# Kernel optimization log

Hardware: AMD Instinct MI355X
Metric: run time of the kernel (lower is better)

## Reference

```python
import jax, jax.numpy as jnp
import numpy as np

B, H, T, D = 2, 16, 2048, 64
BASE_WINDOW = 256
FULL = 999999


def _make_window_sizes(num_heads=H, base_window=BASE_WINDOW):
    ws = []
    for h in range(num_heads):
        if h < num_heads // 4:
            ws.append(base_window)
        elif h < num_heads // 2:
            ws.append(base_window * 2)
        elif h < 3 * num_heads // 4:
            ws.append(base_window * 4)
        else:
            ws.append(FULL)
    return jnp.asarray(ws, dtype=jnp.int32)


def setup_inputs() -> dict:
    key = jax.random.key(0)
    kq, kk, kv = jax.random.split(key, 3)
    Q = jax.random.normal(kq, (B, H, T, D), dtype=jnp.float32)
    K = jax.random.normal(kk, (B, H, T, D), dtype=jnp.float32)
    V = jax.random.normal(kv, (B, H, T, D), dtype=jnp.float32)
    return {"Q": Q, "K": K, "V": V, "window_sizes": _make_window_sizes()}


def reference(Q, K, V, window_sizes):
    b, h, t, d = Q.shape
    scale = 1.0 / np.sqrt(d).astype(np.float32)
    idx = jnp.arange(t, dtype=jnp.int32)
    diff = idx[:, None] - idx[None, :]  # [T, T], q_idx - kv_idx
    # causal & |q-k| <= w  ==  0 <= diff <= w  (per head)
    mask = (diff >= 0) & (diff[None, :, :] <= window_sizes[:, None, None])  # [H, T, T]
    scores = jnp.einsum('bhqd,bhkd->bhqk', Q, K) * scale  # [B, H, T, T]
    scores = jnp.where(mask[None], scores, -jnp.inf)
    attn = jax.nn.softmax(scores, axis=-1)
    return jnp.einsum('bhqk,bhkd->bhqd', attn, V)
```

## Files before the change

kernel.cpp:

```cpp
#include <hip/hip_runtime.h>
#include <hip/hip_bf16.h>


constexpr int Bc = 2, Hc = 16, Tc = 2048, Dc = 64;
constexpr int BQ = 64;
constexpr int BK = 32;
constexpr float QSCALE = 0.125f * 1.44269504088896340736f;
constexpr float CMAX = 16.0f;

constexpr size_t KB_OFF = 256;
constexpr size_t VB_OFF = 256 + (size_t)Bc * Hc * Tc * Dc * 2;
constexpr int HEADE = Tc * Dc;

typedef __attribute__((ext_vector_type(8))) short short8;
typedef __attribute__((ext_vector_type(4))) float float4v;
typedef __attribute__((ext_vector_type(2))) unsigned int uint2v;

#if defined(__has_builtin)
#if __has_builtin(__builtin_amdgcn_exp2f)
#define EXP2 __builtin_amdgcn_exp2f
#endif
#endif
#ifndef EXP2
#define EXP2 exp2f
#endif

__device__ inline unsigned f2bf_u(float f) {
    union { float f; unsigned u; } v; v.f = f;
    return (v.u + 0x7fffu + ((v.u >> 16) & 1u)) >> 16;
}

__device__ inline short8 pack8(const float* t) {
    short8 r;
#pragma unroll
    for (int j = 0; j < 8; j++) r[j] = (short)f2bf_u(t[j]);
    return r;
}

__device__ inline unsigned pk_bf16(float a, float b) {
    __hip_bfloat162 h = __float22bfloat162_rn(make_float2(a, b));
    union { __hip_bfloat162 h; unsigned u; } v; v.h = h;
    return v.u;
}

__device__ inline short8 mk8(unsigned a0, unsigned a1, unsigned a2, unsigned a3) {
    union { unsigned u[4]; short8 s; } v;
    v.u[0] = a0; v.u[1] = a1; v.u[2] = a2; v.u[3] = a3;
    return v.s;
}

__global__ __launch_bounds__(256)
void preconv_kernel(const float* __restrict__ K, const float* __restrict__ V,
                    unsigned short* __restrict__ Kb, unsigned short* __restrict__ Vtb) {
    const int blk = blockIdx.x;
    const int tid = threadIdx.x;
    if (blk < 2048) {
        const int base = blk * 2048 + tid * 8;
        float4v a = *(const float4v*)(K + base);
        float4v b = *(const float4v*)(K + base + 4);
        float t[8] = {a[0], a[1], a[2], a[3], b[0], b[1], b[2], b[3]};
        *(short8*)(Kb + base) = pack8(t);
    } else {
        __shared__ float tile[64][65];
        const int blk2 = blk - 2048;
        const int bh = blk2 >> 5;
        const int t0 = (blk2 & 31) * 64;
        const float* src = V + (size_t)bh * HEADE + (size_t)t0 * Dc;
#pragma unroll
        for (int i = 0; i < 4; i++) {
            const int r = (tid >> 4) + i * 16;
            const int d4 = (tid & 15) * 4;
            float4v v4 = *(const float4v*)(src + r * Dc + d4);
            tile[r][d4] = v4[0]; tile[r][d4 + 1] = v4[1];
            tile[r][d4 + 2] = v4[2]; tile[r][d4 + 3] = v4[3];
        }
        __syncthreads();
        unsigned short* dst = Vtb + (size_t)bh * HEADE + t0;
#pragma unroll
        for (int i = 0; i < 2; i++) {
            const int d = (tid >> 3) + 32 * i;
            const int c = tid & 7;
            float t[8];
#pragma unroll
            for (int j = 0; j < 8; j++) t[j] = tile[c * 8 + j][d];
            *(short8*)(dst + (size_t)d * Tc + c * 8) = pack8(t);
        }
    }
}

__global__ __launch_bounds__(256, 4)
void dswa_kernel(const float* __restrict__ Q,
                 const unsigned short* __restrict__ Kb,
                 const unsigned short* __restrict__ Vtb,
                 const int* __restrict__ wsz,
                 float* __restrict__ O) {
    __shared__ __align__(16) unsigned short LDS[18432];

    const int tid  = threadIdx.x;
    const int wave = tid >> 6;
    const int g    = wave >> 1;
    const int wq   = wave & 1;
    const int lane = tid & 63;
    const int quad = lane >> 4;
    const int l16  = lane & 15;

    unsigned short* Kw = &LDS[wave * 4608];
    unsigned short* Vw = &LDS[wave * 4608 + 2048];

    const int krow  = lane >> 1;
    const int kcolh = (lane & 1) * 32;
    const int vrow  = lane;

    const int blk  = blockIdx.x;
    const int ci   = blk & 255;
    const int slot = blk >> 8;
    const int b    = ci & 1;
    const int q5   = (ci >> 1) & 31;
    const int hh   = ci >> 6;
    const int h    = (3 - slot) * 4 + hh;
    const int qt   = (slot == 0) ? q5 : 31 - q5;
    const int q0   = qt * BQ;
    const int win  = wsz[h];

    const size_t headoff = (size_t)(b * Hc + h) * HEADE;
    const float* Qp = Q + headoff;
    const unsigned short* Kbh = Kb + headoff;
    const unsigned short* Vbh = Vtb + headoff;
    float* Op = O + headoff;

    short8 qf[2][2];
#pragma unroll
    for (int s = 0; s < 2; s++) {
        const int qrow = q0 + wq * 32 + s * 16 + l16;
#pragma unroll
        for (int c = 0; c < 2; c++) {
            const float* src = Qp + (size_t)qrow * Dc + c * 32 + quad * 8;
            float4v a = *(const float4v*)src;
            float4v d4 = *(const float4v*)(src + 4);
            float t[8] = {a[0]*QSCALE, a[1]*QSCALE, a[2]*QSCALE, a[3]*QSCALE,
                          d4[0]*QSCALE, d4[1]*QSCALE, d4[2]*QSCALE, d4[3]*QSCALE};
            qf[s][c] = pack8(t);
        }
    }

    float4v acc[2][4];
#pragma unroll
    for (int s = 0; s < 2; s++)
#pragma unroll
        for (int nb = 0; nb < 4; nb++) acc[s][nb] = (float4v){0.f, 0.f, 0.f, 0.f};
    float lp0 = 0.0f, lp1 = 0.0f;

    const int kv_lo = (max(0, q0 - win)) & ~(BK - 1);
    const int C = (q0 + BQ - kv_lo) >> 5;

    const int kv0g = kv_lo + g * BK;
    const unsigned short* kgp = Kbh + (size_t)(kv0g + krow) * Dc + kcolh;
    const unsigned short* vgp = Vbh + (size_t)vrow * Tc + kv0g;

    short8 kr0, kr1, kr2, kr3, vr0, vr1, vr2, vr3;
    if (g < C) {
        kr0 = *(const short8*)(kgp);
        kr1 = *(const short8*)(kgp + 8);
        kr2 = *(const short8*)(kgp + 16);
        kr3 = *(const short8*)(kgp + 24);
        vr0 = *(const short8*)(vgp);
        vr1 = *(const short8*)(vgp + 8);
        vr2 = *(const short8*)(vgp + 16);
        vr3 = *(const short8*)(vgp + 24);
    }
    kgp += 64 * Dc; vgp += 64;

    for (int ti = g; ti < C; ti += 2) {
        const int kv0 = kv_lo + ti * BK;

        {
            const int ks = (krow & 7) << 3;
            *(short8*)&Kw[krow * 64 + ((kcolh)      ^ ks)] = kr0;
            *(short8*)&Kw[krow * 64 + ((kcolh + 8)  ^ ks)] = kr1;
            *(short8*)&Kw[krow * 64 + ((kcolh + 16) ^ ks)] = kr2;
            *(short8*)&Kw[krow * 64 + ((kcolh + 24) ^ ks)] = kr3;
            *(short8*)&Vw[vrow * 40 + 0]  = vr0;
            *(short8*)&Vw[vrow * 40 + 8]  = vr1;
            *(short8*)&Vw[vrow * 40 + 16] = vr2;
            *(short8*)&Vw[vrow * 40 + 24] = vr3;
        }

        if (ti + 2 < C) {
            kr0 = *(const short8*)(kgp);
            kr1 = *(const short8*)(kgp + 8);
            kr2 = *(const short8*)(kgp + 16);
            kr3 = *(const short8*)(kgp + 24);
            vr0 = *(const short8*)(vgp);
            vr1 = *(const short8*)(vgp + 8);
            vr2 = *(const short8*)(vgp + 16);
            vr3 = *(const short8*)(vgp + 24);
        }
        kgp += 64 * Dc; vgp += 64;

        float4v sT0[2], sT1[2];
        __builtin_amdgcn_s_setprio(1);
#pragma unroll
        for (int mb = 0; mb < 2; mb++) {
            float4v c0 = {-CMAX, -CMAX, -CMAX, -CMAX};
            float4v c1 = {-CMAX, -CMAX, -CMAX, -CMAX};
#pragma unroll
            for (int ch = 0; ch < 2; ch++) {
                const int row = mb * 16 + l16;
                short8 kf = *(short8*)&Kw[row * 64 +
                                          ((ch * 32 + quad * 8) ^ ((row & 7) << 3))];
                c0 = __builtin_amdgcn_mfma_f32_16x16x32_bf16(kf, qf[0][ch], c0, 0, 0, 0);
                c1 = __builtin_amdgcn_mfma_f32_16x16x32_bf16(kf, qf[1][ch], c1, 0, 0, 0);
            }
            sT0[mb] = c0; sT1[mb] = c1;
        }
        __builtin_amdgcn_s_setprio(0);

        short8 pf0, pf1;
        {
            const int rs = q0 + wq * 32;
            const bool interior = (kv0 + 31 <= rs) && (rs + 15 - kv0 <= win);
            if (!interior) {
                const int dbase = rs + l16 - kv0 - quad * 4;
#pragma unroll
                for (int mb = 0; mb < 2; mb++)
#pragma unroll
                    for (int r = 0; r < 4; r++) {
                        const unsigned diff = (unsigned)(dbase - mb * 16 - r);
                        sT0[mb][r] = (diff <= (unsigned)win) ? sT0[mb][r] : -3.0e38f;
                    }
            }
            unsigned w[4];
#pragma unroll
            for (int mb = 0; mb < 2; mb++) {
                float p0 = EXP2(sT0[mb][0]);
                float p1 = EXP2(sT0[mb][1]);
                float p2 = EXP2(sT0[mb][2]);
                float p3 = EXP2(sT0[mb][3]);
                lp0 += (p0 + p1) + (p2 + p3);
                w[2 * mb]     = pk_bf16(p0, p1);
                w[2 * mb + 1] = pk_bf16(p2, p3);
            }
            uint2v pa = __builtin_amdgcn_permlane32_swap(w[0], w[2], false, false);
            uint2v c02 = __builtin_amdgcn_permlane16_swap(pa[0], pa[1], false, false);
            uint2v pb = __builtin_amdgcn_permlane32_swap(w[1], w[3], false, false);
            uint2v c13 = __builtin_amdgcn_permlane16_swap(pb[0], pb[1], false, false);
            pf0 = mk8(c02[0], c13[0], c02[1], c13[1]);
        }
        {
            const int rs = q0 + wq * 32 + 16;
            const bool interior = (kv0 + 31 <= rs) && (rs + 15 - kv0 <= win);
            if (!interior) {
                const int dbase = rs + l16 - kv0 - quad * 4;
#pragma unroll
                for (int mb = 0; mb < 2; mb++)
#pragma unroll
                    for (int r = 0; r < 4; r++) {
                        const unsigned diff = (unsigned)(dbase - mb * 16 - r);
                        sT1[mb][r] = (diff <= (unsigned)win) ? sT1[mb][r] : -3.0e38f;
                    }
            }
            unsigned w[4];
#pragma unroll
            for (int mb = 0; mb < 2; mb++) {
                float p0 = EXP2(sT1[mb][0]);
                float p1 = EXP2(sT1[mb][1]);
                float p2 = EXP2(sT1[mb][2]);
                float p3 = EXP2(sT1[mb][3]);
                lp1 += (p0 + p1) + (p2 + p3);
                w[2 * mb]     = pk_bf16(p0, p1);
                w[2 * mb + 1] = pk_bf16(p2, p3);
            }
            uint2v pa = __builtin_amdgcn_permlane32_swap(w[0], w[2], false, false);
            uint2v c02 = __builtin_amdgcn_permlane16_swap(pa[0], pa[1], false, false);
            uint2v pb = __builtin_amdgcn_permlane32_swap(w[1], w[3], false, false);
            uint2v c13 = __builtin_amdgcn_permlane16_swap(pb[0], pb[1], false, false);
            pf1 = mk8(c02[0], c13[0], c02[1], c13[1]);
        }

        __builtin_amdgcn_s_setprio(1);
#pragma unroll
        for (int nb = 0; nb < 4; nb++) {
            short8 vf = *(short8*)&Vw[(nb * 16 + l16) * 40 + quad * 8];
            acc[0][nb] = __builtin_amdgcn_mfma_f32_16x16x32_bf16(pf0, vf, acc[0][nb], 0, 0, 0);
            acc[1][nb] = __builtin_amdgcn_mfma_f32_16x16x32_bf16(pf1, vf, acc[1][nb], 0, 0, 0);
        }
        __builtin_amdgcn_s_setprio(0);
    }

    lp0 += __shfl_xor(lp0, 16); lp0 += __shfl_xor(lp0, 32);
    lp1 += __shfl_xor(lp1, 16); lp1 += __shfl_xor(lp1, 32);

    __syncthreads();
    float* fl = (float*)LDS;
    if (g == 1) {
#pragma unroll
        for (int s = 0; s < 2; s++) {
            if (quad == 0) fl[(wq * 32 + s * 16 + l16) * 66 + 64] = (s ? lp1 : lp0);
#pragma unroll
            for (int r = 0; r < 4; r++) {
                const int row = wq * 32 + s * 16 + quad * 4 + r;
#pragma unroll
                for (int nb = 0; nb < 4; nb++)
                    fl[row * 66 + nb * 16 + l16] = acc[s][nb][r];
            }
        }
    }
    __syncthreads();
    if (g == 0) {
#pragma unroll
        for (int s = 0; s < 2; s++) {
            const float lps = s ? lp1 : lp0;
#pragma unroll
            for (int r = 0; r < 4; r++) {
                const int row = wq * 32 + s * 16 + quad * 4 + r;
                const float l0 = __shfl(lps, quad * 4 + r);
                const float lt = l0 + fl[row * 66 + 64];
                const float inv = 1.0f / lt;
                float* dst = Op + (size_t)(q0 + row) * Dc;
#pragma unroll
                for (int nb = 0; nb < 4; nb++)
                    dst[nb * 16 + l16] = (acc[s][nb][r] + fl[row * 66 + nb * 16 + l16]) * inv;
            }
        }
    }
}

extern "C" void kernel_launch(void* const* d_in, const int* in_sizes, int n_in,
                              void* d_out, int out_size, void* d_ws, size_t ws_size,
                              hipStream_t stream) {
    (void)in_sizes; (void)n_in; (void)ws_size; (void)out_size;
    const float* Q = (const float*)d_in[0];
    const float* K = (const float*)d_in[1];
    const float* V = (const float*)d_in[2];
    const int* wsz = (const int*)d_in[3];
    float* Out = (float*)d_out;

    unsigned short* Kb  = (unsigned short*)((char*)d_ws + KB_OFF);
    unsigned short* Vtb = (unsigned short*)((char*)d_ws + VB_OFF);

    preconv_kernel<<<dim3(3072), dim3(256), 0, stream>>>(K, V, Kb, Vtb);
    dswa_kernel<<<dim3(1024), dim3(256), 0, stream>>>(Q, Kb, Vtb, wsz, Out);
}
```

Baseline: 140.1 us.

## Load K and V MFMA fragments directly from global memory, bypassing LDS

Drops the per-wave LDS staging of K and V tiles. MFMA operand fragments are now loaded straight from global memory (K prefetched one iteration ahead, V loaded right after the QK MFMAs), and LDS shrinks to just the final reduction buffer. This removes the LDS write/read round trip and its latency, and the smaller LDS footprint may allow higher occupancy. In exchange the global loads are smaller and less coalesced (16-byte pieces scattered across rows), and V load latency is now exposed inside the iteration rather than hidden by a full-tile prefetch.

Result: no change. 141.0 us (+0.6%).

```diff
diff --git a/kernel.cpp b/kernel.cpp
--- a/kernel.cpp
+++ b/kernel.cpp
@@ -94,7 +94,7 @@
                  const unsigned short* __restrict__ Vtb,
                  const int* __restrict__ wsz,
                  float* __restrict__ O) {
-    __shared__ __align__(16) unsigned short LDS[18432];
+    __shared__ __align__(16) float fl[4224];
 
     const int tid  = threadIdx.x;
     const int wave = tid >> 6;
@@ -103,13 +103,6 @@
     const int lane = tid & 63;
     const int quad = lane >> 4;
     const int l16  = lane & 15;
-
-    unsigned short* Kw = &LDS[wave * 4608];
-    unsigned short* Vw = &LDS[wave * 4608 + 2048];
-
-    const int krow  = lane >> 1;
-    const int kcolh = (lane & 1) * 32;
-    const int vrow  = lane;
 
     const int blk  = blockIdx.x;
     const int ci   = blk & 255;
@@ -153,67 +146,51 @@
     const int kv_lo = (max(0, q0 - win)) & ~(BK - 1);
     const int C = (q0 + BQ - kv_lo) >> 5;
 
-    const int kv0g = kv_lo + g * BK;
-    const unsigned short* kgp = Kbh + (size_t)(kv0g + krow) * Dc + kcolh;
-    const unsigned short* vgp = Vbh + (size_t)vrow * Tc + kv0g;
-
-    short8 kr0, kr1, kr2, kr3, vr0, vr1, vr2, vr3;
-    if (g < C) {
-        kr0 = *(const short8*)(kgp);
-        kr1 = *(const short8*)(kgp + 8);
-        kr2 = *(const short8*)(kgp + 16);
-        kr3 = *(const short8*)(kgp + 24);
-        vr0 = *(const short8*)(vgp);
-        vr1 = *(const short8*)(vgp + 8);
-        vr2 = *(const short8*)(vgp + 16);
-        vr3 = *(const short8*)(vgp + 24);
-    }
-    kgp += 64 * Dc; vgp += 64;
+    const unsigned short* kbase = Kbh + (size_t)l16 * Dc + quad * 8;
+    const unsigned short* vbase = Vbh + (size_t)l16 * Tc + quad * 8;
+
+    short8 k0, k1, k2, k3;
+    {
+        const unsigned short* kp = kbase + (size_t)(kv_lo + g * BK) * Dc;
+        k0 = *(const short8*)(kp);
+        k1 = *(const short8*)(kp + 16 * Dc);
+        k2 = *(const short8*)(kp + 32);
+        k3 = *(const short8*)(kp + 16 * Dc + 32);
+    }
 
     for (int ti = g; ti < C; ti += 2) {
         const int kv0 = kv_lo + ti * BK;
 
-        {
-            const int ks = (krow & 7) << 3;
-            *(short8*)&Kw[krow * 64 + ((kcolh)      ^ ks)] = kr0;
-            *(short8*)&Kw[krow * 64 + ((kcolh + 8)  ^ ks)] = kr1;
-            *(short8*)&Kw[krow * 64 + ((kcolh + 16) ^ ks)] = kr2;
-            *(short8*)&Kw[krow * 64 + ((kcolh + 24) ^ ks)] = kr3;
-            *(short8*)&Vw[vrow * 40 + 0]  = vr0;
-            *(short8*)&Vw[vrow * 40 + 8]  = vr1;
-            *(short8*)&Vw[vrow * 40 + 16] = vr2;
-            *(short8*)&Vw[vrow * 40 + 24] = vr3;
-        }
-
-        if (ti + 2 < C) {
-            kr0 = *(const short8*)(kgp);
-            kr1 = *(const short8*)(kgp + 8);
-            kr2 = *(const short8*)(kgp + 16);
-            kr3 = *(const short8*)(kgp + 24);
-            vr0 = *(const short8*)(vgp);
-            vr1 = *(const short8*)(vgp + 8);
-            vr2 = *(const short8*)(vgp + 16);
-            vr3 = *(const short8*)(vgp + 24);
-        }
-        kgp += 64 * Dc; vgp += 64;
-
         float4v sT0[2], sT1[2];
         __builtin_amdgcn_s_setprio(1);
-#pragma unroll
-        for (int mb = 0; mb < 2; mb++) {
+        {
             float4v c0 = {-CMAX, -CMAX, -CMAX, -CMAX};
-            float4v c1 = {-CMAX, -CMAX, -CMAX, -CMAX};
-#pragma unroll
-            for (int ch = 0; ch < 2; ch++) {
-                const int row = mb * 16 + l16;
-                short8 kf = *(short8*)&Kw[row * 64 +
-                                          ((ch * 32 + quad * 8) ^ ((row & 7) << 3))];
-                c0 = __builtin_amdgcn_mfma_f32_16x16x32_bf16(kf, qf[0][ch], c0, 0, 0, 0);
-                c1 = __builtin_amdgcn_mfma_f32_16x16x32_bf16(kf, qf[1][ch], c1, 0, 0, 0);
-            }
-            sT0[mb] = c0; sT1[mb] = c1;
+            float4v c1 = c0, c2 = c0, c3 = c0;
+            c0 = __builtin_amdgcn_mfma_f32_16x16x32_bf16(k0, qf[0][0], c0, 0, 0, 0);
+            c1 = __builtin_amdgcn_mfma_f32_16x16x32_bf16(k0, qf[1][0], c1, 0, 0, 0);
+            c2 = __builtin_amdgcn_mfma_f32_16x16x32_bf16(k1, qf[0][0], c2, 0, 0, 0);
+            c3 = __builtin_amdgcn_mfma_f32_16x16x32_bf16(k1, qf[1][0], c3, 0, 0, 0);
+            c0 = __builtin_amdgcn_mfma_f32_16x16x32_bf16(k2, qf[0][1], c0, 0, 0, 0);
+            c1 = __builtin_amdgcn_mfma_f32_16x16x32_bf16(k2, qf[1][1], c1, 0, 0, 0);
+            c2 = __builtin_amdgcn_mfma_f32_16x16x32_bf16(k3, qf[0][1], c2, 0, 0, 0);
+            c3 = __builtin_amdgcn_mfma_f32_16x16x32_bf16(k3, qf[1][1], c3, 0, 0, 0);
+            sT0[0] = c0; sT1[0] = c1; sT0[1] = c2; sT1[1] = c3;
         }
         __builtin_amdgcn_s_setprio(0);
+
+        const unsigned short* vp = vbase + kv0;
+        short8 vf0 = *(const short8*)(vp);
+        short8 vf1 = *(const short8*)(vp + 16 * Tc);
+        short8 vf2 = *(const short8*)(vp + 32 * Tc);
+        short8 vf3 = *(const short8*)(vp + 48 * Tc);
+
+        if (ti + 2 < C) {
+            const unsigned short* kp = kbase + (size_t)(kv0 + 2 * BK) * Dc;
+            k0 = *(const short8*)(kp);
+            k1 = *(const short8*)(kp + 16 * Dc);
+            k2 = *(const short8*)(kp + 32);
+            k3 = *(const short8*)(kp + 16 * Dc + 32);
+        }
 
         short8 pf0, pf1;
         {
@@ -278,12 +255,14 @@
         }
 
         __builtin_amdgcn_s_setprio(1);
-#pragma unroll
-        for (int nb = 0; nb < 4; nb++) {
-            short8 vf = *(short8*)&Vw[(nb * 16 + l16) * 40 + quad * 8];
-            acc[0][nb] = __builtin_amdgcn_mfma_f32_16x16x32_bf16(pf0, vf, acc[0][nb], 0, 0, 0);
-            acc[1][nb] = __builtin_amdgcn_mfma_f32_16x16x32_bf16(pf1, vf, acc[1][nb], 0, 0, 0);
-        }
+        acc[0][0] = __builtin_amdgcn_mfma_f32_16x16x32_bf16(pf0, vf0, acc[0][0], 0, 0, 0);
+        acc[1][0] = __builtin_amdgcn_mfma_f32_16x16x32_bf16(pf1, vf0, acc[1][0], 0, 0, 0);
+        acc[0][1] = __builtin_amdgcn_mfma_f32_16x16x32_bf16(pf0, vf1, acc[0][1], 0, 0, 0);
+        acc[1][1] = __builtin_amdgcn_mfma_f32_16x16x32_bf16(pf1, vf1, acc[1][1], 0, 0, 0);
+        acc[0][2] = __builtin_amdgcn_mfma_f32_16x16x32_bf16(pf0, vf2, acc[0][2], 0, 0, 0);
+        acc[1][2] = __builtin_amdgcn_mfma_f32_16x16x32_bf16(pf1, vf2, acc[1][2], 0, 0, 0);
+        acc[0][3] = __builtin_amdgcn_mfma_f32_16x16x32_bf16(pf0, vf3, acc[0][3], 0, 0, 0);
+        acc[1][3] = __builtin_amdgcn_mfma_f32_16x16x32_bf16(pf1, vf3, acc[1][3], 0, 0, 0);
         __builtin_amdgcn_s_setprio(0);
     }
 
@@ -291,7 +270,6 @@
     lp1 += __shfl_xor(lp1, 16); lp1 += __shfl_xor(lp1, 32);
 
     __syncthreads();
-    float* fl = (float*)LDS;
     if (g == 1) {
 #pragma unroll
         for (int s = 0; s < 2; s++) {
```
